# Performance work log

Hardware: AMD Instinct MI355X
Metric: run time of the kernel (lower is better)

## Reference

```python
import jax, jax.numpy as jnp
import numpy as np

N_NODES = 50000
N_EDGES = 800000
QRY = 128
KEY = 128
VAL = 128
HEADS = 8
HEAD_FEATS = VAL // HEADS
BN_EPS = 1e-5


def setup_inputs() -> dict:
    key = jax.random.key(0)
    ks = jax.random.split(key, 12)
    inp = {
        "ft_q": jax.random.normal(ks[0], (N_NODES, QRY), dtype=jnp.float32),
        "ft_k": jax.random.normal(ks[1], (N_NODES, KEY), dtype=jnp.float32),
        "src": jax.random.randint(ks[2], (N_EDGES,), 0, N_NODES, dtype=jnp.int32),
        "dst": jax.random.randint(ks[3], (N_EDGES,), 0, N_NODES, dtype=jnp.int32),
        # learned params
        "Wq": jax.random.normal(ks[4], (VAL, QRY), dtype=jnp.float32) / np.sqrt(QRY),
        "bq": jnp.zeros((VAL,), dtype=jnp.float32),
        "Wk": jax.random.normal(ks[5], (VAL, KEY), dtype=jnp.float32) / np.sqrt(KEY),
        "Wv": jax.random.normal(ks[6], (VAL, QRY), dtype=jnp.float32) / np.sqrt(QRY),
        "attn_e": jax.random.normal(ks[7], (VAL,), dtype=jnp.float32),
        "bn_q_g": jnp.ones((QRY,), dtype=jnp.float32),
        "bn_q_b": jnp.zeros((QRY,), dtype=jnp.float32),
        "bn_k_g": jnp.ones((KEY,), dtype=jnp.float32),
        "bn_k_b": jnp.zeros((KEY,), dtype=jnp.float32),
    }
    return inp


def _batch_norm(x, gamma, beta):
    # training-mode BatchNorm1d: normalize over batch dim
    mean = jnp.mean(x, axis=0, keepdims=True)
    var = jnp.var(x, axis=0, keepdims=True)
    return (x - mean) * jax.lax.rsqrt(var + BN_EPS) * gamma + beta


def reference(ft_q, ft_k, src, dst, Wq, bq, Wk, Wv, attn_e,
              bn_q_g, bn_q_b, bn_k_g, bn_k_b):
    ft_q = _batch_norm(ft_q, bn_q_g, bn_q_b)
    ft_k = _batch_norm(ft_k, bn_k_g, bn_k_b)

    q = ft_q @ Wq.T + bq                      # [N, VAL]
    k = ft_k @ Wk.T                           # [N, VAL]
    v = (ft_q @ Wv.T).reshape(-1, HEADS, HEAD_FEATS)  # [N, H, D]

    # u_add_v: per-edge e = q[src] + k[dst]
    e = q[src] + k[dst]                       # [E, VAL]
    e = (attn_e * jax.nn.sigmoid(e)).reshape(-1, HEADS, HEAD_FEATS).sum(-1)  # [E, H]

    # edge_softmax grouped by destination node
    m = jax.ops.segment_max(e, dst, num_segments=N_NODES)   # [N, H]
    ex = jnp.exp(e - m[dst])                                # [E, H]
    s = jax.ops.segment_sum(ex, dst, num_segments=N_NODES)  # [N, H]
    a = ex / s[dst]                                         # [E, H]

    # u_mul_e_sum: scatter-sum of v[src] * a over destination
    msg = v[src] * a[:, :, None]                            # [E, H, D]
    rst = jax.ops.segment_sum(msg, dst, num_segments=N_NODES)  # [N, H, D]
    return rst.reshape(-1, VAL)
```

## Files before the change

### kernel.cpp

```cpp
#include <hip/hip_runtime.h>

#define N_NODES 50000
#define N_EDGES 800000
#define FEATS 128
#define NCHUNK 196
#define CPAD 50176
#define GEMM_BX 196
#define GEMM_BLOCKS 588
#define SCAT_BLOCKS 3125
#define NTILE 782
#define NF_WAVES 8192
#define STAT_BLOCKS 256
#define HIST_BLOCKS 512

typedef __attribute__((ext_vector_type(8))) short bf16x8;
typedef __attribute__((ext_vector_type(4))) float f32x4;

__device__ __forceinline__ unsigned short f2bf(float f){
  unsigned u = __float_as_uint(f);
  u += 0x7FFF + ((u >> 16) & 1);
  return (unsigned short)(u >> 16);
}
__device__ __forceinline__ void unpack8(uint4 p, float* f){
  f[0]=__uint_as_float(p.x << 16); f[1]=__uint_as_float(p.x & 0xffff0000u);
  f[2]=__uint_as_float(p.y << 16); f[3]=__uint_as_float(p.y & 0xffff0000u);
  f[4]=__uint_as_float(p.z << 16); f[5]=__uint_as_float(p.z & 0xffff0000u);
  f[6]=__uint_as_float(p.w << 16); f[7]=__uint_as_float(p.w & 0xffff0000u);
}

__global__ __launch_bounds__(256) void stats_hist_kernel(
    const float* __restrict__ ftq, const float* __restrict__ ftk,
    float* __restrict__ sums, const int* __restrict__ dstE,
    int* __restrict__ counts, int* __restrict__ csums,
    unsigned short* __restrict__ rankE){
  __shared__ float red[4*FEATS];
  __shared__ int lchunk[NCHUNK];
  int tid = threadIdx.x, bid = blockIdx.x;
  if (bid < STAT_BLOCKS){
    for (int i = tid; i < 4*FEATS; i += 256) red[i] = 0.f;
    __syncthreads();
    int sub = tid >> 5, c4 = tid & 31;
    const float* Xs = (sub < 4) ? ftq : ftk;
    int so = (sub < 4) ? 0 : 2*FEATS;
    float a0=0,a1=0,a2=0,a3=0,b0=0,b1=0,b2=0,b3=0;
    #pragma unroll 4
    for (int r = bid*4 + (sub&3); r < N_NODES; r += STAT_BLOCKS*4){
      float4 x = *(const float4*)(Xs + (size_t)r*FEATS + c4*4);
      a0+=x.x; b0+=x.x*x.x; a1+=x.y; b1+=x.y*x.y;
      a2+=x.z; b2+=x.z*x.z; a3+=x.w; b3+=x.w*x.w;
    }
    a0 += __shfl_xor(a0,32); a1 += __shfl_xor(a1,32);
    a2 += __shfl_xor(a2,32); a3 += __shfl_xor(a3,32);
    b0 += __shfl_xor(b0,32); b1 += __shfl_xor(b1,32);
    b2 += __shfl_xor(b2,32); b3 += __shfl_xor(b3,32);
    if ((tid & 63) < 32){
      int c0 = c4*4;
      atomicAdd(&red[so + c0+0], a0); atomicAdd(&red[so + c0+1], a1);
      atomicAdd(&red[so + c0+2], a2); atomicAdd(&red[so + c0+3], a3);
      atomicAdd(&red[so + FEATS + c0+0], b0); atomicAdd(&red[so + FEATS + c0+1], b1);
      atomicAdd(&red[so + FEATS + c0+2], b2); atomicAdd(&red[so + FEATS + c0+3], b3);
    }
    __syncthreads();
    for (int i = tid; i < 4*FEATS; i += 256) atomicAdd(&sums[i], red[i]);
  } else {
    for (int i = tid; i < NCHUNK; i += 256) lchunk[i] = 0;
    __syncthreads();
    for (int t = (bid-STAT_BLOCKS)*256 + tid; t < N_EDGES; t += HIST_BLOCKS*256){
      int d = dstE[t];
      int p = atomicAdd(&counts[d], 1);
      rankE[t] = (unsigned short)p;
      atomicAdd(&lchunk[d >> 8], 1);
    }
    __syncthreads();
    for (int i = tid; i < NCHUNK; i += 256)
      if (lchunk[i]) atomicAdd(&csums[i], lchunk[i]);
  }
}

__global__ __launch_bounds__(256) void scan_fold_kernel(
    const int* __restrict__ counts, const int* __restrict__ csums,
    int* __restrict__ loc, int* __restrict__ bscan,
    const float* __restrict__ Wq, const float* __restrict__ bq,
    const float* __restrict__ Wk, const float* __restrict__ Wv,
    const float* __restrict__ gq, const float* __restrict__ bqn,
    const float* __restrict__ gk, const float* __restrict__ bkn,
    const float* __restrict__ sums,
    unsigned short* __restrict__ Wb, float* __restrict__ bias){
  __shared__ int s[256];
  int tid = threadIdx.x, bid = blockIdx.x;
  if (bid < NCHUNK){
    int i = bid*256 + tid;
    int v = counts[i];
    s[tid] = v; __syncthreads();
    for (int d = 1; d < 256; d <<= 1){
      int tv = (tid >= d) ? s[tid-d] : 0; __syncthreads();
      s[tid] += tv; __syncthreads();
    }
    loc[i] = s[tid] - v;
  } else if (bid == NCHUNK){
    int v = (tid < NCHUNK) ? csums[tid] : 0;
    s[tid] = v; __syncthreads();
    for (int d = 1; d < 256; d <<= 1){
      int tv = (tid >= d) ? s[tid-d] : 0; __syncthreads();
      s[tid] += tv; __syncthreads();
    }
    if (tid < NCHUNK) bscan[tid] = s[tid] - v;
  } else {
    int wv = (bid - NCHUNK - 1)*4 + (tid >> 6);
    int lane = tid & 63;
    int m = wv >> 7;
    int o = wv & 127;
    const float* Wsrc = (m==0) ? Wq : (m==1) ? Wv : Wk;
    const float* g   = (m==2) ? gk : gq;
    const float* bb  = (m==2) ? bkn : bqn;
    const float* s0  = (m==2) ? (sums + 2*FEATS) : sums;
    const float invN = 1.0f / (float)N_NODES;
    float acc = 0.f;
    unsigned short w2[2];
    int i0 = lane*2;
    #pragma unroll
    for (int t = 0; t < 2; t++){
      int i = i0 + t;
      float mean = s0[i]*invN;
      float var  = s0[FEATS+i]*invN - mean*mean;
      float rstd = rsqrtf(var + 1e-5f);
      float scale = g[i]*rstd;
      float shift = bb[i] - mean*scale;
      float w = Wsrc[o*FEATS + i];
      w2[t] = f2bf(w*scale);
      acc += shift*w;
    }
    ((unsigned*)Wb)[(m*FEATS*FEATS + o*FEATS + i0) >> 1] =
        (unsigned)w2[0] | ((unsigned)w2[1] << 16);
    #pragma unroll
    for (int off = 1; off < 64; off <<= 1) acc += __shfl_xor(acc, off);
    if (lane == 0) bias[m*FEATS + o] = acc + ((m==0) ? bq[o] : 0.f);
  }
}

__global__ __launch_bounds__(256) void gemm_scatter_kernel(
    const float* __restrict__ ftq, const float* __restrict__ ftk,
    const unsigned short* __restrict__ Wball, const float* __restrict__ biasall,
    unsigned short* __restrict__ qv, unsigned short* __restrict__ kb,
    const int* __restrict__ dstE, const int* __restrict__ srcE,
    const int* __restrict__ loc, const int* __restrict__ bscan,
    const unsigned short* __restrict__ rankE, int* __restrict__ src_csr){
  __shared__ unsigned short Bs[FEATS][136];
  int tid = threadIdx.x, bid = blockIdx.x;
  if (bid >= GEMM_BLOCKS){
    int t = (bid - GEMM_BLOCKS)*256 + tid;
    int d = dstE[t];
    src_csr[loc[d] + bscan[d >> 8] + (int)rankE[t]] = srcE[t];
    return;
  }
  int m = bid / GEMM_BX;
  int bx = bid - m*GEMM_BX;
  const float* X = (m==2) ? ftk : ftq;
  {
    const uint4* srcp = (const uint4*)(Wball + m*FEATS*FEATS);
    for (int idx = tid; idx < FEATS*FEATS/8; idx += 256){
      int n = idx >> 4;
      int kk = (idx & 15) * 8;
      *(uint4*)&Bs[n][kk] = srcp[idx];
    }
  }
  __syncthreads();
  int wave = tid >> 6, lane = tid & 63;
  int mrow = lane & 15, quad = lane >> 4;
  unsigned short* Out = (m==2) ? kb : (qv + m*128);
  const int ostride = (m==2) ? FEATS : 256;
  float bv[8];
  #pragma unroll
  for (int ct = 0; ct < 8; ct++) bv[ct] = biasall[m*FEATS + ct*16 + mrow];
  float4 cur[8], nxt[8];
  auto loadx = [&](float4* buf, int t){
    int arow = t*64 + wave*16 + mrow;
    bool rok = arow < N_NODES;
    const float* xp = X + (size_t)(rok ? arow : 0)*FEATS + quad*8;
    #pragma unroll
    for (int kt = 0; kt < 4; kt++){
      float4 x0 = *(const float4*)(xp + kt*32);
      float4 x1 = *(const float4*)(xp + kt*32 + 4);
      if (!rok){ x0 = make_float4(0.f,0.f,0.f,0.f); x1 = x0; }
      buf[2*kt] = x0; buf[2*kt+1] = x1;
    }
  };
  loadx(cur, bx);
  for (int t = bx; t < NTILE; t += GEMM_BX){
    int tn = t + GEMM_BX;
    if (tn < NTILE) loadx(nxt, tn);
    f32x4 acc[8];
    #pragma unroll
    for (int i = 0; i < 8; i++) acc[i] = (f32x4){0.f,0.f,0.f,0.f};
    #pragma unroll
    for (int kt = 0; kt < 4; kt++){
      float4 x0 = cur[2*kt], x1 = cur[2*kt+1];
      bf16x8 a;
      a[0]=(short)f2bf(x0.x); a[1]=(short)f2bf(x0.y); a[2]=(short)f2bf(x0.z); a[3]=(short)f2bf(x0.w);
      a[4]=(short)f2bf(x1.x); a[5]=(short)f2bf(x1.y); a[6]=(short)f2bf(x1.z); a[7]=(short)f2bf(x1.w);
      int kbk = kt*32 + quad*8;
      #pragma unroll
      for (int ct = 0; ct < 8; ct++){
        bf16x8 b = *(bf16x8*)&Bs[ct*16 + mrow][kbk];
        acc[ct] = __builtin_amdgcn_mfma_f32_16x16x32_bf16(a, b, acc[ct], 0, 0, 0);
      }
    }
    int row0 = t*64;
    #pragma unroll
    for (int ct = 0; ct < 8; ct++){
      int col = ct*16 + mrow;
      #pragma unroll
      for (int v = 0; v < 4; v++){
        int orow = row0 + wave*16 + quad*4 + v;
        unsigned ub = f2bf(acc[ct][v] + bv[ct]);
        unsigned partner = (unsigned)__shfl_xor((int)ub, 1);
        if (!(mrow & 1) && orow < N_NODES)
          *(unsigned*)&Out[(size_t)orow*ostride + col] = ub | (partner << 16);
      }
    }
    #pragma unroll
    for (int i = 0; i < 8; i++) cur[i] = nxt[i];
  }
}

__global__ __launch_bounds__(256) void node_fused_kernel(
    const unsigned short* __restrict__ qv, const unsigned short* __restrict__ kb,
    const float* __restrict__ attn, const int* __restrict__ src_csr,
    const int* __restrict__ loc, const int* __restrict__ bscan,
    float* __restrict__ out){
  int tid = threadIdx.x;
  int lane = tid & 63;
  int h = lane & 7, g = lane >> 3;
  int w = blockIdx.x*4 + (tid >> 6);
  const float L2E = 1.44269504f;
  float ar[16];
  {
    const uint4* ap = (const uint4*)(attn + h*16);
    uint4 a0 = ap[0], a1 = ap[1], a2 = ap[2], a3 = ap[3];
    ar[0]=__uint_as_float(a0.x); ar[1]=__uint_as_float(a0.y); ar[2]=__uint_as_float(a0.z); ar[3]=__uint_as_float(a0.w);
    ar[4]=__uint_as_float(a1.x); ar[5]=__uint_as_float(a1.y); ar[6]=__uint_as_float(a1.z); ar[7]=__uint_as_float(a1.w);
    ar[8]=__uint_as_float(a2.x); ar[9]=__uint_as_float(a2.y); ar[10]=__uint_as_float(a2.z); ar[11]=__uint_as_float(a2.w);
    ar[12]=__uint_as_float(a3.x); ar[13]=__uint_as_float(a3.y); ar[14]=__uint_as_float(a3.z); ar[15]=__uint_as_float(a3.w);
  }
  for (int n = w; n < N_NODES; n += NF_WAVES){
    int off0 = loc[n]   + bscan[n>>8];
    int off1 = loc[n+1] + bscan[(n+1)>>8];
    int deg = off1 - off0;
    if (deg == 0){
      ((float2*)(out + (size_t)n*FEATS))[lane] = make_float2(0.f, 0.f);
      continue;
    }
    float kf2[16];
    {
      const unsigned short* kr = kb + (size_t)n*FEATS + h*16;
      uint4 k0 = *(const uint4*)kr;
      uint4 k1 = *(const uint4*)(kr + 8);
      float kf[16]; unpack8(k0, kf); unpack8(k1, kf+8);
      #pragma unroll
      for (int i = 0; i < 16; i++) kf2[i] = -L2E * kf[i];
    }
    float ssum = 0.f;
    float acc[16];
    #pragma unroll
    for (int i = 0; i < 16; i++) acc[i] = 0.f;
    if (g < deg){
      int sA = src_csr[off0 + g];
      int jB = g + 8;
      int sB = (jB < deg) ? src_csr[off0 + jB] : sA;
      const unsigned short* pA = qv + (size_t)sA*256 + h*16;
      uint4 qa0 = *(const uint4*)pA;
      uint4 qa1 = *(const uint4*)(pA + 8);
      while (true){
        uint4 va0 = *(const uint4*)(pA + 128);
        uint4 va1 = *(const uint4*)(pA + 136);
        const unsigned short* pB = qv + (size_t)sB*256 + h*16;
        uint4 qb0 = *(const uint4*)pB;
        uint4 qb1 = *(const uint4*)(pB + 8);
        int jC = jB + 8;
        int sC = (jC < deg) ? src_csr[off0 + jC] : sB;
        float qf[16]; unpack8(qa0, qf); unpack8(qa1, qf+8);
        float t = 0.f;
        #pragma unroll
        for (int i = 0; i < 16; i++){
          float xs = fmaf(qf[i], -L2E, kf2[i]);
          float sg = __builtin_amdgcn_rcpf(1.f + __builtin_amdgcn_exp2f(xs));
          t = fmaf(ar[i], sg, t);
        }
        float ex = __builtin_amdgcn_exp2f(t * L2E);
        ssum += ex;
        float vf[16]; unpack8(va0, vf); unpack8(va1, vf+8);
        #pragma unroll
        for (int i = 0; i < 16; i++) acc[i] = fmaf(ex, vf[i], acc[i]);
        if (jB >= deg) break;
        qa0 = qb0; qa1 = qb1; pA = pB;
        jB = jC; sB = sC;
      }
    }
    ssum += __shfl_xor(ssum, 8); ssum += __shfl_xor(ssum, 16); ssum += __shfl_xor(ssum, 32);
    #pragma unroll
    for (int i = 0; i < 16; i++){
      acc[i] += __shfl_xor(acc[i], 8);
      acc[i] += __shfl_xor(acc[i], 16);
      acc[i] += __shfl_xor(acc[i], 32);
    }
    if (g == 0){
      float inv_s = 1.f / ssum;
      float4* op = (float4*)(out + (size_t)n*FEATS + h*16);
      op[0] = make_float4(acc[0]*inv_s, acc[1]*inv_s, acc[2]*inv_s, acc[3]*inv_s);
      op[1] = make_float4(acc[4]*inv_s, acc[5]*inv_s, acc[6]*inv_s, acc[7]*inv_s);
      op[2] = make_float4(acc[8]*inv_s, acc[9]*inv_s, acc[10]*inv_s, acc[11]*inv_s);
      op[3] = make_float4(acc[12]*inv_s, acc[13]*inv_s, acc[14]*inv_s, acc[15]*inv_s);
    }
  }
}

extern "C" void kernel_launch(void* const* d_in, const int* in_sizes, int n_in,
                              void* d_out, int out_size, void* d_ws, size_t ws_size,
                              hipStream_t stream){
  (void)in_sizes; (void)n_in; (void)out_size; (void)ws_size;
  const float* ftq  = (const float*)d_in[0];
  const float* ftk  = (const float*)d_in[1];
  const int*   srcE = (const int*)d_in[2];
  const int*   dstE = (const int*)d_in[3];
  const float* Wq   = (const float*)d_in[4];
  const float* bq   = (const float*)d_in[5];
  const float* Wk   = (const float*)d_in[6];
  const float* Wv   = (const float*)d_in[7];
  const float* attn = (const float*)d_in[8];
  const float* gq   = (const float*)d_in[9];
  const float* bqn  = (const float*)d_in[10];
  const float* gk   = (const float*)d_in[11];
  const float* bkn  = (const float*)d_in[12];

  char* ws = (char*)d_ws;
  int*   counts  = (int*)(ws + 0);
  float* sums    = (float*)(ws + 200704);
  int*   csums   = (int*)(ws + 202752);
  int*   loc     = (int*)(ws + 203536);
  int*   bscan   = (int*)(ws + 404240);
  int*   src_csr = (int*)(ws + 405024);
  unsigned short* rankE = (unsigned short*)(ws + 3605024);
  unsigned short* Wb = (unsigned short*)(ws + 5205024);
  float* biasf   = (float*)(ws + 5303328);
  unsigned short* qv = (unsigned short*)(ws + 5304864);
  unsigned short* kb = qv + (size_t)N_NODES*256;
  float* out = (float*)d_out;

  hipMemsetAsync(ws, 0, 203536, stream);

  hipLaunchKernelGGL(stats_hist_kernel, dim3(STAT_BLOCKS + HIST_BLOCKS), dim3(256), 0, stream,
                     ftq, ftk, sums, dstE, counts, csums, rankE);
  hipLaunchKernelGGL(scan_fold_kernel, dim3(293), dim3(256), 0, stream,
                     counts, csums, loc, bscan,
                     Wq, bq, Wk, Wv, gq, bqn, gk, bkn, sums, Wb, biasf);
  hipLaunchKernelGGL(gemm_scatter_kernel, dim3(GEMM_BLOCKS + SCAT_BLOCKS), dim3(256), 0, stream,
                     ftq, ftk, Wb, biasf, qv, kb, dstE, srcE, loc, bscan, rankE, src_csr);
  hipLaunchKernelGGL(node_fused_kernel, dim3(NF_WAVES/4), dim3(256), 0, stream,
                     qv, kb, attn, src_csr, loc, bscan, out);
}
```

Before: 277.0 us.

## Use atomic work queue for node batches and hardware bf16 pack conversion

The node kernel now claims batches of four destination nodes from a global atomic counter instead of a fixed grid-stride loop. This evens out per-wave load, since node degrees vary. The counter is initialised inside the scatter part of the preceding kernel, and the workspace offsets shift to make room for it. The GEMM also replaces the software float-to-bf16 rounding with the v_cvt_pk_bf16_f32 instruction, which cuts VALU work. The cost is one atomic per batch per wave and a dependency on a counter that only the previous kernel resets.

```diff
diff --git a/kernel.cpp b/kernel.cpp
--- a/kernel.cpp
+++ b/kernel.cpp
@@ -10,16 +10,23 @@
 #define SCAT_BLOCKS 3125
 #define NTILE 782
 #define NF_WAVES 8192
+#define NF_BATCH 4
 #define STAT_BLOCKS 256
 #define HIST_BLOCKS 512
 
 typedef __attribute__((ext_vector_type(8))) short bf16x8;
 typedef __attribute__((ext_vector_type(4))) float f32x4;
+typedef union { uint4 u; bf16x8 v; } pack8;
 
 __device__ __forceinline__ unsigned short f2bf(float f){
   unsigned u = __float_as_uint(f);
   u += 0x7FFF + ((u >> 16) & 1);
   return (unsigned short)(u >> 16);
+}
+__device__ __forceinline__ unsigned cvtpk(float lo, float hi){
+  unsigned r;
+  asm("v_cvt_pk_bf16_f32 %0, %1, %2" : "=v"(r) : "v"(lo), "v"(hi));
+  return r;
 }
 __device__ __forceinline__ void unpack8(uint4 p, float* f){
   f[0]=__uint_as_float(p.x << 16); f[1]=__uint_as_float(p.x & 0xffff0000u);
@@ -144,10 +151,13 @@
     unsigned short* __restrict__ qv, unsigned short* __restrict__ kb,
     const int* __restrict__ dstE, const int* __restrict__ srcE,
     const int* __restrict__ loc, const int* __restrict__ bscan,
-    const unsigned short* __restrict__ rankE, int* __restrict__ src_csr){
+    const unsigned short* __restrict__ rankE, int* __restrict__ src_csr,
+    int* __restrict__ nodecur){
   __shared__ unsigned short Bs[FEATS][136];
   int tid = threadIdx.x, bid = blockIdx.x;
   if (bid >= GEMM_BLOCKS){
+    if (bid == GEMM_BLOCKS && tid == 0)
+      *nodecur = NF_WAVES*NF_BATCH;
     int t = (bid - GEMM_BLOCKS)*256 + tid;
     int d = dstE[t];
     src_csr[loc[d] + bscan[d >> 8] + (int)rankE[t]] = srcE[t];
@@ -195,14 +205,14 @@
     #pragma unroll
     for (int kt = 0; kt < 4; kt++){
       float4 x0 = cur[2*kt], x1 = cur[2*kt+1];
-      bf16x8 a;
-      a[0]=(short)f2bf(x0.x); a[1]=(short)f2bf(x0.y); a[2]=(short)f2bf(x0.z); a[3]=(short)f2bf(x0.w);
-      a[4]=(short)f2bf(x1.x); a[5]=(short)f2bf(x1.y); a[6]=(short)f2bf(x1.z); a[7]=(short)f2bf(x1.w);
+      pack8 a;
+      a.u.x = cvtpk(x0.x, x0.y); a.u.y = cvtpk(x0.z, x0.w);
+      a.u.z = cvtpk(x1.x, x1.y); a.u.w = cvtpk(x1.z, x1.w);
       int kbk = kt*32 + quad*8;
       #pragma unroll
       for (int ct = 0; ct < 8; ct++){
         bf16x8 b = *(bf16x8*)&Bs[ct*16 + mrow][kbk];
-        acc[ct] = __builtin_amdgcn_mfma_f32_16x16x32_bf16(a, b, acc[ct], 0, 0, 0);
+        acc[ct] = __builtin_amdgcn_mfma_f32_16x16x32_bf16(a.v, b, acc[ct], 0, 0, 0);
       }
     }
     int row0 = t*64;
@@ -227,7 +237,7 @@
     const unsigned short* __restrict__ qv, const unsigned short* __restrict__ kb,
     const float* __restrict__ attn, const int* __restrict__ src_csr,
     const int* __restrict__ loc, const int* __restrict__ bscan,
-    float* __restrict__ out){
+    int* __restrict__ nodecur, float* __restrict__ out){
   int tid = threadIdx.x;
   int lane = tid & 63;
   int h = lane & 7, g = lane >> 3;
@@ -242,75 +252,82 @@
     ar[8]=__uint_as_float(a2.x); ar[9]=__uint_as_float(a2.y); ar[10]=__uint_as_float(a2.z); ar[11]=__uint_as_float(a2.w);
     ar[12]=__uint_as_float(a3.x); ar[13]=__uint_as_float(a3.y); ar[14]=__uint_as_float(a3.z); ar[15]=__uint_as_float(a3.w);
   }
-  for (int n = w; n < N_NODES; n += NF_WAVES){
-    int off0 = loc[n]   + bscan[n>>8];
-    int off1 = loc[n+1] + bscan[(n+1)>>8];
-    int deg = off1 - off0;
-    if (deg == 0){
-      ((float2*)(out + (size_t)n*FEATS))[lane] = make_float2(0.f, 0.f);
-      continue;
-    }
-    float kf2[16];
-    {
-      const unsigned short* kr = kb + (size_t)n*FEATS + h*16;
-      uint4 k0 = *(const uint4*)kr;
-      uint4 k1 = *(const uint4*)(kr + 8);
-      float kf[16]; unpack8(k0, kf); unpack8(k1, kf+8);
+  int base = w*NF_BATCH;
+  while (base < N_NODES){
+    int nb0 = 0;
+    if (lane == 0) nb0 = atomicAdd(nodecur, NF_BATCH);
+    int nend = base + NF_BATCH; if (nend > N_NODES) nend = N_NODES;
+    for (int n = base; n < nend; ++n){
+      int off0 = loc[n]   + bscan[n>>8];
+      int off1 = loc[n+1] + bscan[(n+1)>>8];
+      int deg = off1 - off0;
+      if (deg == 0){
+        ((float2*)(out + (size_t)n*FEATS))[lane] = make_float2(0.f, 0.f);
+        continue;
+      }
+      float kf2[16];
+      {
+        const unsigned short* kr = kb + (size_t)n*FEATS + h*16;
+        uint4 k0 = *(const uint4*)kr;
+        uint4 k1 = *(const uint4*)(kr + 8);
+        float kf[16]; unpack8(k0, kf); unpack8(k1, kf+8);
+        #pragma unroll
+        for (int i = 0; i < 16; i++) kf2[i] = -L2E * kf[i];
+      }
+      float ssum = 0.f;
+      float acc[16];
       #pragma unroll
-      for (int i = 0; i < 16; i++) kf2[i] = -L2E * kf[i];
-    }
-    float ssum = 0.f;
-    float acc[16];
-    #pragma unroll
-    for (int i = 0; i < 16; i++) acc[i] = 0.f;
-    if (g < deg){
-      int sA = src_csr[off0 + g];
-      int jB = g + 8;
-      int sB = (jB < deg) ? src_csr[off0 + jB] : sA;
-      const unsigned short* pA = qv + (size_t)sA*256 + h*16;
-      uint4 qa0 = *(const uint4*)pA;
-      uint4 qa1 = *(const uint4*)(pA + 8);
-      while (true){
-        uint4 va0 = *(const uint4*)(pA + 128);
-        uint4 va1 = *(const uint4*)(pA + 136);
-        const unsigned short* pB = qv + (size_t)sB*256 + h*16;
-        uint4 qb0 = *(const uint4*)pB;
-        uint4 qb1 = *(const uint4*)(pB + 8);
-        int jC = jB + 8;
-        int sC = (jC < deg) ? src_csr[off0 + jC] : sB;
-        float qf[16]; unpack8(qa0, qf); unpack8(qa1, qf+8);
-        float t = 0.f;
-        #pragma unroll
-        for (int i = 0; i < 16; i++){
-          float xs = fmaf(qf[i], -L2E, kf2[i]);
-          float sg = __builtin_amdgcn_rcpf(1.f + __builtin_amdgcn_exp2f(xs));
-          t = fmaf(ar[i], sg, t);
+      for (int i = 0; i < 16; i++) acc[i] = 0.f;
+      if (g < deg){
+        int sA = src_csr[off0 + g];
+        int jB = g + 8;
+        int sB = (jB < deg) ? src_csr[off0 + jB] : sA;
+        const unsigned short* pA = qv + (size_t)sA*256 + h*16;
+        uint4 qa0 = *(const uint4*)pA;
+        uint4 qa1 = *(const uint4*)(pA + 8);
+        while (true){
+          uint4 va0 = *(const uint4*)(pA + 128);
+          uint4 va1 = *(const uint4*)(pA + 136);
+          const unsigned short* pB = qv + (size_t)sB*256 + h*16;
+          uint4 qb0 = *(const uint4*)pB;
+          uint4 qb1 = *(const uint4*)(pB + 8);
+          int jC = jB + 8;
+          int sC = (jC < deg) ? src_csr[off0 + jC] : sB;
+          float qf[16]; unpack8(qa0, qf); unpack8(qa1, qf+8);
+          float t = 0.f;
+          #pragma unroll
+          for (int i = 0; i < 16; i++){
+            float xs = fmaf(qf[i], -L2E, kf2[i]);
+            float sg = __builtin_amdgcn_rcpf(1.f + __builtin_amdgcn_exp2f(xs));
+            t = fmaf(ar[i], sg, t);
+          }
+          float ex = __builtin_amdgcn_exp2f(t * L2E);
+          ssum += ex;
+          float vf[16]; unpack8(va0, vf); unpack8(va1, vf+8);
+          #pragma unroll
+          for (int i = 0; i < 16; i++) acc[i] = fmaf(ex, vf[i], acc[i]);
+          if (jB >= deg) break;
+          qa0 = qb0; qa1 = qb1; pA = pB;
+          jB = jC; sB = sC;
         }
-        float ex = __builtin_amdgcn_exp2f(t * L2E);
-        ssum += ex;
-        float vf[16]; unpack8(va0, vf); unpack8(va1, vf+8);
-        #pragma unroll
-        for (int i = 0; i < 16; i++) acc[i] = fmaf(ex, vf[i], acc[i]);
-        if (jB >= deg) break;
-        qa0 = qb0; qa1 = qb1; pA = pB;
-        jB = jC; sB = sC;
-      }
-    }
-    ssum += __shfl_xor(ssum, 8); ssum += __shfl_xor(ssum, 16); ssum += __shfl_xor(ssum, 32);
-    #pragma unroll
-    for (int i = 0; i < 16; i++){
-      acc[i] += __shfl_xor(acc[i], 8);
-      acc[i] += __shfl_xor(acc[i], 16);
-      acc[i] += __shfl_xor(acc[i], 32);
-    }
-    if (g == 0){
-      float inv_s = 1.f / ssum;
-      float4* op = (float4*)(out + (size_t)n*FEATS + h*16);
-      op[0] = make_float4(acc[0]*inv_s, acc[1]*inv_s, acc[2]*inv_s, acc[3]*inv_s);
-      op[1] = make_float4(acc[4]*inv_s, acc[5]*inv_s, acc[6]*inv_s, acc[7]*inv_s);
-      op[2] = make_float4(acc[8]*inv_s, acc[9]*inv_s, acc[10]*inv_s, acc[11]*inv_s);
-      op[3] = make_float4(acc[12]*inv_s, acc[13]*inv_s, acc[14]*inv_s, acc[15]*inv_s);
-    }
+      }
+      ssum += __shfl_xor(ssum, 8); ssum += __shfl_xor(ssum, 16); ssum += __shfl_xor(ssum, 32);
+      #pragma unroll
+      for (int i = 0; i < 16; i++){
+        acc[i] += __shfl_xor(acc[i], 8);
+        acc[i] += __shfl_xor(acc[i], 16);
+        acc[i] += __shfl_xor(acc[i], 32);
+      }
+      if (g == 0){
+        float inv_s = 1.f / ssum;
+        float4* op = (float4*)(out + (size_t)n*FEATS + h*16);
+        op[0] = make_float4(acc[0]*inv_s, acc[1]*inv_s, acc[2]*inv_s, acc[3]*inv_s);
+        op[1] = make_float4(acc[4]*inv_s, acc[5]*inv_s, acc[6]*inv_s, acc[7]*inv_s);
+        op[2] = make_float4(acc[8]*inv_s, acc[9]*inv_s, acc[10]*inv_s, acc[11]*inv_s);
+        op[3] = make_float4(acc[12]*inv_s, acc[13]*inv_s, acc[14]*inv_s, acc[15]*inv_s);
+      }
+    }
+    base = __shfl(nb0, 0);
   }
 }
 
@@ -336,13 +353,14 @@
   int*   counts  = (int*)(ws + 0);
   float* sums    = (float*)(ws + 200704);
   int*   csums   = (int*)(ws + 202752);
-  int*   loc     = (int*)(ws + 203536);
-  int*   bscan   = (int*)(ws + 404240);
-  int*   src_csr = (int*)(ws + 405024);
-  unsigned short* rankE = (unsigned short*)(ws + 3605024);
-  unsigned short* Wb = (unsigned short*)(ws + 5205024);
-  float* biasf   = (float*)(ws + 5303328);
-  unsigned short* qv = (unsigned short*)(ws + 5304864);
+  int*   nodecur = (int*)(ws + 203536);
+  int*   loc     = (int*)(ws + 203552);
+  int*   bscan   = (int*)(ws + 404256);
+  int*   src_csr = (int*)(ws + 405040);
+  unsigned short* rankE = (unsigned short*)(ws + 3605040);
+  unsigned short* Wb = (unsigned short*)(ws + 5205040);
+  float* biasf   = (float*)(ws + 5303344);
+  unsigned short* qv = (unsigned short*)(ws + 5304880);
   unsigned short* kb = qv + (size_t)N_NODES*256;
   float* out = (float*)d_out;
 
@@ -354,7 +372,7 @@
                      counts, csums, loc, bscan,
                      Wq, bq, Wk, Wv, gq, bqn, gk, bkn, sums, Wb, biasf);
   hipLaunchKernelGGL(gemm_scatter_kernel, dim3(GEMM_BLOCKS + SCAT_BLOCKS), dim3(256), 0, stream,
-                     ftq, ftk, Wb, biasf, qv, kb, dstE, srcE, loc, bscan, rankE, src_csr);
+                     ftq, ftk, Wb, biasf, qv, kb, dstE, srcE, loc, bscan, rankE, src_csr, nodecur);
   hipLaunchKernelGGL(node_fused_kernel, dim3(NF_WAVES/4), dim3(256), 0, stream,
-                     qv, kb, attn, src_csr, loc, bscan, out);
-}
+                     qv, kb, attn, src_csr, loc, bscan, nodecur, out);
+}
```

Measured after the change: 371.3 us. +34.0%, slower.

## Fuse Q and V projections over a shared bf16 input and swizzle LDS weights

Applied to the files above, without the earlier changes.

While computing BN statistics, the stats kernel also writes a bf16 copy of ft_q. The GEMM kernel then computes the Q and V projections in one block that loads each A tile once and runs it against two weight planes, so ft_q is no longer read twice in fp32 and the GEMM grid shrinks. The LDS weight tiles are XOR-swizzled instead of padded, bf16 conversion uses the packed hardware convert instruction, and the per-edge sigmoid dot product in the node kernel is split across four accumulators for more ILP. In exchange, the stats kernel writes an extra bf16 buffer, each Q/V block needs twice the LDS and more accumulator registers, and padded tail rows read unmasked garbage from the bf16 buffer, which is only safe because those output rows are masked.

```diff
diff --git a/kernel.cpp b/kernel.cpp
--- a/kernel.cpp
+++ b/kernel.cpp
@@ -6,7 +6,7 @@
 #define NCHUNK 196
 #define CPAD 50176
 #define GEMM_BX 196
-#define GEMM_BLOCKS 588
+#define GEMM_BLOCKS 392
 #define SCAT_BLOCKS 3125
 #define NTILE 782
 #define NF_WAVES 8192
@@ -15,11 +15,17 @@
 
 typedef __attribute__((ext_vector_type(8))) short bf16x8;
 typedef __attribute__((ext_vector_type(4))) float f32x4;
+typedef union { uint4 u; bf16x8 v; } pack8;
 
 __device__ __forceinline__ unsigned short f2bf(float f){
   unsigned u = __float_as_uint(f);
   u += 0x7FFF + ((u >> 16) & 1);
   return (unsigned short)(u >> 16);
+}
+__device__ __forceinline__ unsigned cvtpk(float lo, float hi){
+  unsigned r;
+  asm("v_cvt_pk_bf16_f32 %0, %1, %2" : "=v"(r) : "v"(lo), "v"(hi));
+  return r;
 }
 __device__ __forceinline__ void unpack8(uint4 p, float* f){
   f[0]=__uint_as_float(p.x << 16); f[1]=__uint_as_float(p.x & 0xffff0000u);
@@ -32,7 +38,7 @@
     const float* __restrict__ ftq, const float* __restrict__ ftk,
     float* __restrict__ sums, const int* __restrict__ dstE,
     int* __restrict__ counts, int* __restrict__ csums,
-    unsigned short* __restrict__ rankE){
+    unsigned short* __restrict__ rankE, unsigned short* __restrict__ xqb){
   __shared__ float red[4*FEATS];
   __shared__ int lchunk[NCHUNK];
   int tid = threadIdx.x, bid = blockIdx.x;
@@ -42,10 +48,13 @@
     int sub = tid >> 5, c4 = tid & 31;
     const float* Xs = (sub < 4) ? ftq : ftk;
     int so = (sub < 4) ? 0 : 2*FEATS;
+    bool isq = (sub < 4);
     float a0=0,a1=0,a2=0,a3=0,b0=0,b1=0,b2=0,b3=0;
     #pragma unroll 4
     for (int r = bid*4 + (sub&3); r < N_NODES; r += STAT_BLOCKS*4){
       float4 x = *(const float4*)(Xs + (size_t)r*FEATS + c4*4);
+      if (isq)
+        *(uint2*)&xqb[(size_t)r*FEATS + c4*4] = make_uint2(cvtpk(x.x,x.y), cvtpk(x.z,x.w));
       a0+=x.x; b0+=x.x*x.x; a1+=x.y; b1+=x.y*x.y;
       a2+=x.z; b2+=x.z*x.z; a3+=x.w; b3+=x.w*x.w;
     }
@@ -139,13 +148,13 @@
 }
 
 __global__ __launch_bounds__(256) void gemm_scatter_kernel(
-    const float* __restrict__ ftq, const float* __restrict__ ftk,
+    const unsigned short* __restrict__ xqb, const float* __restrict__ ftk,
     const unsigned short* __restrict__ Wball, const float* __restrict__ biasall,
     unsigned short* __restrict__ qv, unsigned short* __restrict__ kb,
     const int* __restrict__ dstE, const int* __restrict__ srcE,
     const int* __restrict__ loc, const int* __restrict__ bscan,
     const unsigned short* __restrict__ rankE, int* __restrict__ src_csr){
-  __shared__ unsigned short Bs[FEATS][136];
+  __shared__ unsigned short Bs[2][FEATS][FEATS];
   int tid = threadIdx.x, bid = blockIdx.x;
   if (bid >= GEMM_BLOCKS){
     int t = (bid - GEMM_BLOCKS)*256 + tid;
@@ -153,73 +162,96 @@
     src_csr[loc[d] + bscan[d >> 8] + (int)rankE[t]] = srcE[t];
     return;
   }
-  int m = bid / GEMM_BX;
-  int bx = bid - m*GEMM_BX;
-  const float* X = (m==2) ? ftk : ftq;
+  int isk = (bid >= GEMM_BX);
+  int bx = isk ? bid - GEMM_BX : bid;
+  int nplanes = isk ? 1 : 2;
   {
-    const uint4* srcp = (const uint4*)(Wball + m*FEATS*FEATS);
-    for (int idx = tid; idx < FEATS*FEATS/8; idx += 256){
-      int n = idx >> 4;
-      int kk = (idx & 15) * 8;
-      *(uint4*)&Bs[n][kk] = srcp[idx];
+    for (int p = 0; p < nplanes; p++){
+      int m = isk ? 2 : p;
+      const uint4* srcp = (const uint4*)(Wball + m*FEATS*FEATS);
+      for (int idx = tid; idx < FEATS*FEATS/8; idx += 256){
+        int n = idx >> 4, ck = idx & 15;
+        *(uint4*)&Bs[p][n][(ck ^ (n & 15))*8] = srcp[idx];
+      }
     }
   }
   __syncthreads();
   int wave = tid >> 6, lane = tid & 63;
   int mrow = lane & 15, quad = lane >> 4;
-  unsigned short* Out = (m==2) ? kb : (qv + m*128);
-  const int ostride = (m==2) ? FEATS : 256;
-  float bv[8];
+  float bv[2][8];
   #pragma unroll
-  for (int ct = 0; ct < 8; ct++) bv[ct] = biasall[m*FEATS + ct*16 + mrow];
-  float4 cur[8], nxt[8];
-  auto loadx = [&](float4* buf, int t){
+  for (int p = 0; p < 2; p++)
+    #pragma unroll
+    for (int ct = 0; ct < 8; ct++)
+      bv[p][ct] = biasall[(isk ? 2 : p)*FEATS + ct*16 + mrow];
+  uint4 cur[4], nxt[4];
+  auto loadA = [&](uint4* buf, int t){
     int arow = t*64 + wave*16 + mrow;
-    bool rok = arow < N_NODES;
-    const float* xp = X + (size_t)(rok ? arow : 0)*FEATS + quad*8;
-    #pragma unroll
-    for (int kt = 0; kt < 4; kt++){
-      float4 x0 = *(const float4*)(xp + kt*32);
-      float4 x1 = *(const float4*)(xp + kt*32 + 4);
-      if (!rok){ x0 = make_float4(0.f,0.f,0.f,0.f); x1 = x0; }
-      buf[2*kt] = x0; buf[2*kt+1] = x1;
+    if (!isk){
+      const unsigned short* xp = xqb + (size_t)arow*FEATS + quad*8;
+      buf[0] = *(const uint4*)xp;
+      buf[1] = *(const uint4*)(xp + 32);
+      buf[2] = *(const uint4*)(xp + 64);
+      buf[3] = *(const uint4*)(xp + 96);
+    } else {
+      bool rok = arow < N_NODES;
+      const float* xp = ftk + (size_t)(rok ? arow : 0)*FEATS + quad*8;
+      #pragma unroll
+      for (int kt = 0; kt < 4; kt++){
+        float4 x0 = *(const float4*)(xp + kt*32);
+        float4 x1 = *(const float4*)(xp + kt*32 + 4);
+        if (!rok){ x0 = make_float4(0.f,0.f,0.f,0.f); x1 = x0; }
+        buf[kt].x = cvtpk(x0.x, x0.y); buf[kt].y = cvtpk(x0.z, x0.w);
+        buf[kt].z = cvtpk(x1.x, x1.y); buf[kt].w = cvtpk(x1.z, x1.w);
+      }
     }
   };
-  loadx(cur, bx);
+  loadA(cur, bx);
   for (int t = bx; t < NTILE; t += GEMM_BX){
     int tn = t + GEMM_BX;
-    if (tn < NTILE) loadx(nxt, tn);
-    f32x4 acc[8];
-    #pragma unroll
-    for (int i = 0; i < 8; i++) acc[i] = (f32x4){0.f,0.f,0.f,0.f};
+    if (tn < NTILE) loadA(nxt, tn);
+    f32x4 acc[2][8];
+    #pragma unroll
+    for (int p = 0; p < 2; p++)
+      #pragma unroll
+      for (int i = 0; i < 8; i++) acc[p][i] = (f32x4){0.f,0.f,0.f,0.f};
     #pragma unroll
     for (int kt = 0; kt < 4; kt++){
-      float4 x0 = cur[2*kt], x1 = cur[2*kt+1];
-      bf16x8 a;
-      a[0]=(short)f2bf(x0.x); a[1]=(short)f2bf(x0.y); a[2]=(short)f2bf(x0.z); a[3]=(short)f2bf(x0.w);
-      a[4]=(short)f2bf(x1.x); a[5]=(short)f2bf(x1.y); a[6]=(short)f2bf(x1.z); a[7]=(short)f2bf(x1.w);
-      int kbk = kt*32 + quad*8;
+      pack8 a; a.u = cur[kt];
       #pragma unroll
       for (int ct = 0; ct < 8; ct++){
-        bf16x8 b = *(bf16x8*)&Bs[ct*16 + mrow][kbk];
-        acc[ct] = __builtin_amdgcn_mfma_f32_16x16x32_bf16(a, b, acc[ct], 0, 0, 0);
+        bf16x8 b0 = *(bf16x8*)&Bs[0][ct*16 + mrow][((kt*4 + quad) ^ mrow)*8];
+        acc[0][ct] = __builtin_amdgcn_mfma_f32_16x16x32_bf16(a.v, b0, acc[0][ct], 0, 0, 0);
+      }
+      if (!isk){
+        #pragma unroll
+        for (int ct = 0; ct < 8; ct++){
+          bf16x8 b1 = *(bf16x8*)&Bs[1][ct*16 + mrow][((kt*4 + quad) ^ mrow)*8];
+          acc[1][ct] = __builtin_amdgcn_mfma_f32_16x16x32_bf16(a.v, b1, acc[1][ct], 0, 0, 0);
+        }
       }
     }
     int row0 = t*64;
     #pragma unroll
-    for (int ct = 0; ct < 8; ct++){
-      int col = ct*16 + mrow;
-      #pragma unroll
-      for (int v = 0; v < 4; v++){
-        int orow = row0 + wave*16 + quad*4 + v;
-        unsigned ub = f2bf(acc[ct][v] + bv[ct]);
-        unsigned partner = (unsigned)__shfl_xor((int)ub, 1);
-        if (!(mrow & 1) && orow < N_NODES)
-          *(unsigned*)&Out[(size_t)orow*ostride + col] = ub | (partner << 16);
-      }
-    }
-    #pragma unroll
-    for (int i = 0; i < 8; i++) cur[i] = nxt[i];
+    for (int p = 0; p < 2; p++){
+      if (isk && p) break;
+      unsigned short* Out = isk ? kb : (qv + p*128);
+      const int ostride = isk ? FEATS : 256;
+      #pragma unroll
+      for (int ct = 0; ct < 8; ct++){
+        int col = ct*16 + mrow;
+        #pragma unroll
+        for (int v = 0; v < 4; v++){
+          int orow = row0 + wave*16 + quad*4 + v;
+          float s = acc[p][ct][v] + bv[p][ct];
+          float pf = __shfl_xor(s, 1);
+          if (!(mrow & 1) && orow < N_NODES)
+            *(unsigned*)&Out[(size_t)orow*ostride + col] = cvtpk(s, pf);
+        }
+      }
+    }
+    #pragma unroll
+    for (int i = 0; i < 4; i++) cur[i] = nxt[i];
   }
 }
 
@@ -279,13 +311,19 @@
         int jC = jB + 8;
         int sC = (jC < deg) ? src_csr[off0 + jC] : sB;
         float qf[16]; unpack8(qa0, qf); unpack8(qa1, qf+8);
-        float t = 0.f;
+        float ta = 0.f, tb = 0.f, tc = 0.f, td = 0.f;
         #pragma unroll
-        for (int i = 0; i < 16; i++){
-          float xs = fmaf(qf[i], -L2E, kf2[i]);
-          float sg = __builtin_amdgcn_rcpf(1.f + __builtin_amdgcn_exp2f(xs));
-          t = fmaf(ar[i], sg, t);
+        for (int i = 0; i < 16; i += 4){
+          float x0 = fmaf(qf[i+0], -L2E, kf2[i+0]);
+          float x1 = fmaf(qf[i+1], -L2E, kf2[i+1]);
+          float x2 = fmaf(qf[i+2], -L2E, kf2[i+2]);
+          float x3 = fmaf(qf[i+3], -L2E, kf2[i+3]);
+          ta = fmaf(ar[i+0], __builtin_amdgcn_rcpf(1.f + __builtin_amdgcn_exp2f(x0)), ta);
+          tb = fmaf(ar[i+1], __builtin_amdgcn_rcpf(1.f + __builtin_amdgcn_exp2f(x1)), tb);
+          tc = fmaf(ar[i+2], __builtin_amdgcn_rcpf(1.f + __builtin_amdgcn_exp2f(x2)), tc);
+          td = fmaf(ar[i+3], __builtin_amdgcn_rcpf(1.f + __builtin_amdgcn_exp2f(x3)), td);
         }
+        float t = (ta + tb) + (tc + td);
         float ex = __builtin_amdgcn_exp2f(t * L2E);
         ssum += ex;
         float vf[16]; unpack8(va0, vf); unpack8(va1, vf+8);
@@ -342,19 +380,20 @@
   unsigned short* rankE = (unsigned short*)(ws + 3605024);
   unsigned short* Wb = (unsigned short*)(ws + 5205024);
   float* biasf   = (float*)(ws + 5303328);
-  unsigned short* qv = (unsigned short*)(ws + 5304864);
-  unsigned short* kb = qv + (size_t)N_NODES*256;
+  unsigned short* xqb = (unsigned short*)(ws + 5304864);
+  unsigned short* qv  = (unsigned short*)(ws + 18149920);
+  unsigned short* kb  = qv + (size_t)N_NODES*256;
   float* out = (float*)d_out;
 
   hipMemsetAsync(ws, 0, 203536, stream);
 
   hipLaunchKernelGGL(stats_hist_kernel, dim3(STAT_BLOCKS + HIST_BLOCKS), dim3(256), 0, stream,
-                     ftq, ftk, sums, dstE, counts, csums, rankE);
+                     ftq, ftk, sums, dstE, counts, csums, rankE, xqb);
   hipLaunchKernelGGL(scan_fold_kernel, dim3(293), dim3(256), 0, stream,
                      counts, csums, loc, bscan,
                      Wq, bq, Wk, Wv, gq, bqn, gk, bkn, sums, Wb, biasf);
   hipLaunchKernelGGL(gemm_scatter_kernel, dim3(GEMM_BLOCKS + SCAT_BLOCKS), dim3(256), 0, stream,
-                     ftq, ftk, Wb, biasf, qv, kb, dstE, srcE, loc, bscan, rankE, src_csr);
+                     xqb, ftk, Wb, biasf, qv, kb, dstE, srcE, loc, bscan, rankE, src_csr);
   hipLaunchKernelGGL(node_fused_kernel, dim3(NF_WAVES/4), dim3(256), 0, stream,
                      qv, kb, attn, src_csr, loc, bscan, out);
 }
```

Result: no change. 277.6 us (+0.2%).
